# Kernel tuning notes

Hardware: AMD Instinct MI355X
Metric: run time of the kernel (lower is better)

Reference implementation:

```python
import jax, jax.numpy as jnp
import numpy as np

D = 128  # h_dim == in_dim

def _gat_layer(h, d, src, dst, n_dst, W, U, V, a):
    # h: [N_src, Din], d: [E, 1], src/dst: [E]
    z = h @ W.T          # [N_src, D]
    zi = h @ U.T         # [N_src, D]
    t = d @ V.T          # [E, 1]
    Dh = W.shape[0]
    # attn_fc on concat([z_src, z_dst, t]) split into three partial dots
    e = z[src] @ a[:Dh] + z[dst] @ a[Dh:2 * Dh] + t[:, 0] * a[2 * Dh]
    e = jax.nn.leaky_relu(e)  # [E]
    # segment softmax over incoming edges of each dst node
    m = jax.ops.segment_max(e, dst, num_segments=n_dst)
    ex = jnp.exp(e - m[dst])
    s = jax.ops.segment_sum(ex, dst, num_segments=n_dst)
    alpha = ex / s[dst]  # [E]
    zn = jax.ops.segment_sum(alpha[:, None] * z[src], dst, num_segments=n_dst)
    return jax.nn.relu(zi[:n_dst] + zn)


def setup_inputs() -> dict:
    key = jax.random.key(0)
    ks = jax.random.split(key, 16)
    N0, ND0, ND1 = 100000, 40000, 20000
    E0, E1 = 640000, 320000
    sc = 1.0 / np.sqrt(D)
    inp = {
        "attr": jax.random.normal(ks[0], (N0, D), jnp.float32),
        "d0": jax.random.normal(ks[1], (E0, 1), jnp.float32),
        "d1": jax.random.normal(ks[2], (E1, 1), jnp.float32),
        "src0": jax.random.randint(ks[3], (E0,), 0, N0, jnp.int32),
        "dst0": jax.random.randint(ks[4], (E0,), 0, ND0, jnp.int32),
        "src1": jax.random.randint(ks[5], (E1,), 0, ND0, jnp.int32),
        "dst1": jax.random.randint(ks[6], (E1,), 0, ND1, jnp.int32),
        "n_dst0": ND0,
        "n_dst1": ND1,
        "W0": jax.random.normal(ks[7], (D, D), jnp.float32) * sc,
        "U0": jax.random.normal(ks[8], (D, D), jnp.float32) * sc,
        "V0": jax.random.normal(ks[9], (1, 1), jnp.float32),
        "a0": jax.random.normal(ks[10], (2 * D + 1,), jnp.float32) * sc,
        "W1": jax.random.normal(ks[11], (D, D), jnp.float32) * sc,
        "U1": jax.random.normal(ks[12], (D, D), jnp.float32) * sc,
        "V1": jax.random.normal(ks[13], (1, 1), jnp.float32),
        "a1": jax.random.normal(ks[14], (2 * D + 1,), jnp.float32) * sc,
    }
    return inp


def reference(attr, d0, d1, W0, U0, V0, a0, W1, U1, V1, a1,
              src0, dst0, src1, dst1, n_dst0, n_dst1):
    h = _gat_layer(attr, d0, src0, dst0, n_dst0, W0, U0, V0, a0)
    h = _gat_layer(h, d1, src1, dst1, n_dst1, W1, U1, V1, a1)
    return h
```

## Files before the change

kernel.cpp:

```cpp
#include <hip/hip_runtime.h>
#include <math.h>


#define D 128
#define CSTRIDE 32

typedef __bf16 bf16x8 __attribute__((ext_vector_type(8)));
typedef float f32x4 __attribute__((ext_vector_type(4)));

static __device__ __forceinline__ float lrelu(float x) {
  return x >= 0.f ? x : 0.01f * x;
}
static __device__ __forceinline__ unsigned short f2bf(float v) {
  unsigned int u = __float_as_uint(v);
  u += 0x7fffu + ((u >> 16) & 1u);
  return (unsigned short)(u >> 16);
}
static __device__ __forceinline__ float bf2f(unsigned short b) {
  return __uint_as_float((unsigned int)b << 16);
}

static __device__ __forceinline__ float4 loadV4(const float* p) {
  return *(const float4*)p;
}
static __device__ __forceinline__ float4 loadV4(const unsigned short* p) {
  ushort4 t = *(const ushort4*)p;
  return make_float4(bf2f(t.x), bf2f(t.y), bf2f(t.z), bf2f(t.w));
}
static __device__ __forceinline__ void storeV4(float* p, float4 v) {
  *(float4*)p = v;
}
static __device__ __forceinline__ void storeV4(unsigned short* p, float4 v) {
  ushort4 t;
  t.x = f2bf(v.x);
  t.y = f2bf(v.y);
  t.z = f2bf(v.z);
  t.w = f2bf(v.w);
  *(ushort4*)p = t;
}
static __device__ __forceinline__ void storeZi(float* p, float v) { *p = v; }
static __device__ __forceinline__ void storeZi(unsigned short* p, float v) {
  *p = f2bf(v);
}

static __device__ __forceinline__ int swz(int row, int colb) {
  return row * 256 + (colb ^ ((row & 7) << 4));
}

__global__ __launch_bounds__(256) void cvt4_kernel(
    const float* __restrict__ s0, const float* __restrict__ s1,
    const float* __restrict__ s2, const float* __restrict__ s3,
    __bf16* __restrict__ dst) {
  int idx = blockIdx.x * 256 + threadIdx.x;
  const float* s = (idx < 16384) ? s0
                   : (idx < 32768) ? s1
                   : (idx < 49152) ? s2 : s3;
  dst[idx] = (__bf16)s[idx & 16383];
}

__global__ void zero_int_kernel(int* __restrict__ p, int n) {
  int i = blockIdx.x * 256 + threadIdx.x;
  if (i < n) p[i] = 0;
}

static __device__ __forceinline__ void stageA(const float* A, int rblk,
                                              int rlim, int t,
                                              unsigned char* ldsA) {
  const char* base = (const char*)A + (size_t)rblk * 512;
#pragma unroll
  for (int g = 0; g < 8; ++g) {
    int sb = g * 4096 + t * 16;
    float4 v = make_float4(0.f, 0.f, 0.f, 0.f);
    if (rblk + (sb >> 9) < rlim) v = *(const float4*)(base + sb);
    int db = sb >> 1;
    int row = db >> 8, colb = db & 255;
    ushort4 o;
    o.x = f2bf(v.x);
    o.y = f2bf(v.y);
    o.z = f2bf(v.z);
    o.w = f2bf(v.w);
    *(ushort4*)(&ldsA[swz(row, colb)]) = o;
  }
}
static __device__ __forceinline__ void stageA(const unsigned short* A,
                                              int rblk, int rlim, int t,
                                              unsigned char* ldsA) {
  const char* base = (const char*)A + (size_t)rblk * 256;
#pragma unroll
  for (int g = 0; g < 4; ++g) {
    int bi = g * 4096 + t * 16;
    int row = bi >> 8, colb = bi & 255;
    ushort4 lo = {0, 0, 0, 0}, hi = {0, 0, 0, 0};
    if (rblk + row < rlim) {
      lo = *(const ushort4*)(base + bi);
      hi = *(const ushort4*)(base + bi + 8);
    }
    *(ushort4*)(&ldsA[swz(row, colb)]) = lo;
    *(ushort4*)(&ldsA[swz(row, colb) + 8]) = hi;
  }
}

template <typename AT, typename ZiT>
__global__ __launch_bounds__(256, 3) void gemm_lds(
    const AT* __restrict__ A, const __bf16* __restrict__ Wb,
    const __bf16* __restrict__ Ub, unsigned short* __restrict__ z,
    ZiT* __restrict__ zi, const float* __restrict__ a,
    float* __restrict__ zs, float* __restrict__ zd, int n_wb, int rows,
    int ndst) {
  __shared__ unsigned char lds[49152];
  const int t = threadIdx.x;
  const int blk = blockIdx.x;
  const bool isU = (blk >= n_wb);
  const int rblk = (isU ? blk - n_wb : blk) * 64;
  const int rlim = isU ? ndst : rows;
  const __bf16* B = isU ? Ub : Wb;

#pragma unroll
  for (int g = 0; g < 8; ++g) {
    int bi = g * 4096 + t * 16;
    int row = bi >> 8, colb = bi & 255;
    bf16x8 v = *(const bf16x8*)((const char*)B + bi);
    *(bf16x8*)(&lds[swz(row, colb)]) = v;
  }
  stageA(A, rblk, rlim, t, lds + 32768);
  __syncthreads();

  const int wave = t >> 6;
  const int lane = t & 63;
  const int lm = lane & 15;
  const int lk = lane >> 4;
  const int r0 = rblk + wave * 16;
  if (r0 >= rlim) return;

  bf16x8 af[4];
#pragma unroll
  for (int kt = 0; kt < 4; ++kt) {
    int row = wave * 16 + lm;
    af[kt] = *(const bf16x8*)(&lds[32768 + swz(row, kt * 64 + lk * 16)]);
  }

  f32x4 acc[8];
#pragma unroll
  for (int tt = 0; tt < 8; ++tt) acc[tt] = (f32x4){0.f, 0.f, 0.f, 0.f};
#pragma unroll
  for (int kt = 0; kt < 4; ++kt) {
#pragma unroll
    for (int tt = 0; tt < 8; ++tt) {
      int row = tt * 16 + lm;
      bf16x8 bf = *(const bf16x8*)(&lds[swz(row, kt * 64 + lk * 16)]);
      acc[tt] =
          __builtin_amdgcn_mfma_f32_16x16x32_bf16(af[kt], bf, acc[tt], 0, 0, 0);
    }
  }

  if (!isU) {
#pragma unroll
    for (int tt = 0; tt < 8; ++tt)
#pragma unroll
      for (int rr = 0; rr < 4; ++rr)
        z[(size_t)(r0 + lk * 4 + rr) * D + tt * 16 + lm] = f2bf(acc[tt][rr]);

    float p1[4] = {0.f, 0.f, 0.f, 0.f};
    float p2[4] = {0.f, 0.f, 0.f, 0.f};
#pragma unroll
    for (int tt = 0; tt < 8; ++tt) {
      float a1 = a[tt * 16 + lm];
      float a2 = a[D + tt * 16 + lm];
#pragma unroll
      for (int rr = 0; rr < 4; ++rr) {
        p1[rr] += acc[tt][rr] * a1;
        p2[rr] += acc[tt][rr] * a2;
      }
    }
#pragma unroll
    for (int rr = 0; rr < 4; ++rr) {
#pragma unroll
      for (int o = 1; o < 16; o <<= 1) {
        p1[rr] += __shfl_xor(p1[rr], o);
        p2[rr] += __shfl_xor(p2[rr], o);
      }
      if (lm == 0) {
        zs[r0 + lk * 4 + rr] = p1[rr];
        zd[r0 + lk * 4 + rr] = p2[rr];
      }
    }
  } else {
#pragma unroll
    for (int tt = 0; tt < 8; ++tt)
#pragma unroll
      for (int rr = 0; rr < 4; ++rr)
        storeZi(&zi[(size_t)(r0 + lk * 4 + rr) * D + tt * 16 + lm],
                acc[tt][rr]);
  }
}

__global__ void count_rank_kernel(const int* __restrict__ dst0,
                                  const int* __restrict__ dst1,
                                  int* __restrict__ cnt0,
                                  int* __restrict__ cnt1,
                                  int* __restrict__ rank0,
                                  int* __restrict__ rank1, int q0, int q1) {
  int gid = blockIdx.x * 256 + threadIdx.x;
  const int* dst;
  int* cnt;
  int* rank;
  int i0;
  if (gid < q0) {
    dst = dst0; cnt = cnt0; rank = rank0; i0 = gid * 4;
  } else if (gid < q0 + q1) {
    dst = dst1; cnt = cnt1; rank = rank1; i0 = (gid - q0) * 4;
  } else {
    return;
  }
  int4 d4 = *(const int4*)(dst + i0);
  int4 r4;
  r4.x = atomicAdd(&cnt[(size_t)d4.x * CSTRIDE], 1);
  r4.y = atomicAdd(&cnt[(size_t)d4.y * CSTRIDE], 1);
  r4.z = atomicAdd(&cnt[(size_t)d4.z * CSTRIDE], 1);
  r4.w = atomicAdd(&cnt[(size_t)d4.w * CSTRIDE], 1);
  *(int4*)(rank + i0) = r4;
}

__global__ __launch_bounds__(256) void scan_partial2(
    const int* __restrict__ cnt0, const int* __restrict__ cnt1,
    int* __restrict__ part, int nb0, int n0, int n1) {
  __shared__ int sm[4];
  int blk = blockIdx.x;
  const int* cnt;
  int* pt;
  int n, lb;
  if (blk < nb0) {
    cnt = cnt0; pt = part; n = n0; lb = blk;
  } else {
    cnt = cnt1; pt = part + 64; n = n1; lb = blk - nb0;
  }
  int base = lb * 1024;
  int t = threadIdx.x;
  int s = 0;
#pragma unroll
  for (int i = 0; i < 4; ++i) {
    int idx = base + t + i * 256;
    s += (idx < n) ? cnt[(size_t)idx * CSTRIDE] : 0;
  }
  for (int o = 32; o; o >>= 1) s += __shfl_xor(s, o);
  if ((t & 63) == 0) sm[t >> 6] = s;
  __syncthreads();
  if (t == 0) pt[lb] = sm[0] + sm[1] + sm[2] + sm[3];
}

__global__ __launch_bounds__(256) void scan_final2(
    const int* __restrict__ cnt0, const int* __restrict__ cnt1,
    const int* __restrict__ part, int* __restrict__ offs0,
    int* __restrict__ offs1, int nb0, int n0, int n1, int tot0, int tot1) {
  __shared__ int sm[4];
  __shared__ int sbase;
  int blk = blockIdx.x;
  const int* cnt;
  const int* pt;
  int* offs;
  int n, lb, total;
  if (blk < nb0) {
    cnt = cnt0; pt = part; offs = offs0; n = n0; lb = blk; total = tot0;
  } else {
    cnt = cnt1; pt = part + 64; offs = offs1; n = n1; lb = blk - nb0;
    total = tot1;
  }
  int base = lb * 1024;
  int t = threadIdx.x;
  if (t < 64) {
    int v = (t < lb) ? pt[t] : 0;
#pragma unroll
    for (int o = 32; o; o >>= 1) v += __shfl_xor(v, o);
    if (t == 0) sbase = v;
  }
  int idx = base + t * 4;
  int c0 = (idx + 0 < n) ? cnt[(size_t)(idx + 0) * CSTRIDE] : 0;
  int c1 = (idx + 1 < n) ? cnt[(size_t)(idx + 1) * CSTRIDE] : 0;
  int c2 = (idx + 2 < n) ? cnt[(size_t)(idx + 2) * CSTRIDE] : 0;
  int c3 = (idx + 3 < n) ? cnt[(size_t)(idx + 3) * CSTRIDE] : 0;
  int ts = c0 + c1 + c2 + c3;
  int v = ts;
#pragma unroll
  for (int o = 1; o < 64; o <<= 1) {
    int u = __shfl_up(v, o);
    if ((t & 63) >= o) v += u;
  }
  if ((t & 63) == 63) sm[t >> 6] = v;
  __syncthreads();
  int w = t >> 6;
  int waveoff = 0;
  if (w > 0) waveoff += sm[0];
  if (w > 1) waveoff += sm[1];
  if (w > 2) waveoff += sm[2];
  int run = v - ts + waveoff + sbase;
  if (idx + 0 < n) { offs[idx + 0] = run; run += c0; }
  if (idx + 1 < n) { offs[idx + 1] = run; run += c1; }
  if (idx + 2 < n) { offs[idx + 2] = run; run += c2; }
  if (idx + 3 < n) { offs[idx + 3] = run; run += c3; }
  if (lb == 0 && t == 0) offs[n] = total;
}

__global__ void scatter_w_kernel(const int* __restrict__ src,
                                 const int* __restrict__ dst,
                                 const float* __restrict__ dE,
                                 const float* __restrict__ zs,
                                 const float* __restrict__ zd,
                                 const float* __restrict__ V,
                                 const float* __restrict__ a,
                                 const int* __restrict__ rank,
                                 const int* __restrict__ offs,
                                 int2* __restrict__ csr, int E) {
  int i0 = (blockIdx.x * 256 + threadIdx.x) * 4;
  float vc = V[0] * a[2 * D];
  if (i0 + 4 <= E) {
    int4 s4 = *(const int4*)(src + i0);
    int4 d4 = *(const int4*)(dst + i0);
    float4 de = *(const float4*)(dE + i0);
    int4 r4 = *(const int4*)(rank + i0);
    float zs0 = zs[s4.x], zs1 = zs[s4.y], zs2 = zs[s4.z], zs3 = zs[s4.w];
    float zd0 = zd[d4.x], zd1 = zd[d4.y], zd2 = zd[d4.z], zd3 = zd[d4.w];
    int p0 = offs[d4.x] + r4.x;
    int p1 = offs[d4.y] + r4.y;
    int p2 = offs[d4.z] + r4.z;
    int p3 = offs[d4.w] + r4.w;
    float w0 = __expf(lrelu(zs0 + zd0 + de.x * vc));
    float w1 = __expf(lrelu(zs1 + zd1 + de.y * vc));
    float w2 = __expf(lrelu(zs2 + zd2 + de.z * vc));
    float w3 = __expf(lrelu(zs3 + zd3 + de.w * vc));
    csr[p0] = make_int2(s4.x, __float_as_int(w0));
    csr[p1] = make_int2(s4.y, __float_as_int(w1));
    csr[p2] = make_int2(s4.z, __float_as_int(w2));
    csr[p3] = make_int2(s4.w, __float_as_int(w3));
  } else {
    for (int i = i0; i < E; ++i) {
      int di = dst[i];
      int pp = offs[di] + rank[i];
      float w = __expf(lrelu(zs[src[i]] + zd[di] + dE[i] * vc));
      csr[pp] = make_int2(src[i], __float_as_int(w));
    }
  }
}

template <typename OT>
__global__ __launch_bounds__(256) void gat_perdst(
    const unsigned short* __restrict__ z, const int2* __restrict__ csr,
    const int* __restrict__ offs, const OT* __restrict__ ziin,
    OT* __restrict__ hout, int nd) {
  int n = blockIdx.x * 8 + (threadIdx.x >> 5);
  if (n >= nd) return;
  int lane = threadIdx.x & 31;
  int beg = offs[n], end = offs[n + 1];

  float s0 = 0.f, s1 = 0.f;
  float4 acc0 = make_float4(0.f, 0.f, 0.f, 0.f);
  float4 acc1 = make_float4(0.f, 0.f, 0.f, 0.f);
  const unsigned short* zp = z + lane * 4;
  int j = beg;
  for (; j + 8 <= end; j += 8) {
    int2 pr[8];
#pragma unroll
    for (int u = 0; u < 8; ++u) pr[u] = csr[j + u];
    float4 zv[8];
#pragma unroll
    for (int u = 0; u < 8; ++u) zv[u] = loadV4(zp + (size_t)pr[u].x * D);
#pragma unroll
    for (int u = 0; u < 8; u += 2) {
      float wa = __int_as_float(pr[u].y);
      float wb = __int_as_float(pr[u + 1].y);
      s0 += wa;
      acc0.x += wa * zv[u].x;
      acc0.y += wa * zv[u].y;
      acc0.z += wa * zv[u].z;
      acc0.w += wa * zv[u].w;
      s1 += wb;
      acc1.x += wb * zv[u + 1].x;
      acc1.y += wb * zv[u + 1].y;
      acc1.z += wb * zv[u + 1].z;
      acc1.w += wb * zv[u + 1].w;
    }
  }
  for (; j < end; ++j) {
    int2 pr = csr[j];
    float w = __int_as_float(pr.y);
    float4 zv = loadV4(zp + (size_t)pr.x * D);
    s0 += w;
    acc0.x += w * zv.x;
    acc0.y += w * zv.y;
    acc0.z += w * zv.z;
    acc0.w += w * zv.w;
  }
  float s = s0 + s1;
  float inv = (s > 0.f) ? 1.f / s : 0.f;
  float4 acc = make_float4(acc0.x + acc1.x, acc0.y + acc1.y, acc0.z + acc1.z,
                           acc0.w + acc1.w);
  float4 ziv = loadV4(ziin + (size_t)n * D + lane * 4);
  float4 o4;
  o4.x = fmaxf(ziv.x + acc.x * inv, 0.f);
  o4.y = fmaxf(ziv.y + acc.y * inv, 0.f);
  o4.z = fmaxf(ziv.z + acc.z * inv, 0.f);
  o4.w = fmaxf(ziv.w + acc.w * inv, 0.f);
  storeV4(hout + (size_t)n * D + lane * 4, o4);
}

extern "C" void kernel_launch(void* const* d_in, const int* in_sizes, int n_in,
                              void* d_out, int out_size, void* d_ws,
                              size_t ws_size, hipStream_t stream) {
  const float* attr = (const float*)d_in[0];
  const float* d0 = (const float*)d_in[1];
  const float* d1 = (const float*)d_in[2];
  const int* src0 = (const int*)d_in[3];
  const int* dst0 = (const int*)d_in[4];
  const int* src1 = (const int*)d_in[5];
  const int* dst1 = (const int*)d_in[6];
  const float* W0 = (const float*)d_in[9];
  const float* U0 = (const float*)d_in[10];
  const float* V0 = (const float*)d_in[11];
  const float* a0 = (const float*)d_in[12];
  const float* W1 = (const float*)d_in[13];
  const float* U1 = (const float*)d_in[14];
  const float* V1 = (const float*)d_in[15];
  const float* a1 = (const float*)d_in[16];

  const int N0 = in_sizes[0] / D;
  const int E0 = in_sizes[1];
  const int E1 = in_sizes[2];
  const int ND0 = 40000;
  const int ND1 = 20000;

  char* p = (char*)d_ws;
  auto alloc = [&](size_t bytes) {
    char* q = p;
    p += (bytes + 255) & ~(size_t)255;
    return q;
  };
  unsigned short* z = (unsigned short*)alloc((size_t)N0 * D * 2);
  int2* csr = (int2*)alloc((size_t)E0 * 8);
  unsigned short* h1b = (unsigned short*)alloc((size_t)ND0 * D * 2);
  int* rank0 = (int*)alloc((size_t)E0 * 4);
  int* rank1 = (int*)alloc((size_t)E1 * 4);
  float* zs = (float*)alloc((size_t)N0 * 4);
  float* zd = (float*)alloc((size_t)N0 * 4);
  int* offs0 = (int*)alloc((size_t)(ND0 + 1) * 4);
  int* offs1 = (int*)alloc((size_t)(ND1 + 1) * 4);
  int* cnt01 = (int*)alloc((size_t)(ND0 + ND1) * CSTRIDE * 4);
  int* part = (int*)alloc((size_t)128 * 4);
  __bf16* wb = (__bf16*)alloc((size_t)4 * D * D * 2);
  int* cnt0 = cnt01;
  int* cnt1 = cnt01 + (size_t)ND0 * CSTRIDE;
  (void)n_in;
  (void)out_size;
  (void)ws_size;

  float* out = (float*)d_out;

  cvt4_kernel<<<256, 256, 0, stream>>>(W0, U0, W1, U1, wb);
  {
    int ztot = (ND0 + ND1) * CSTRIDE;
    zero_int_kernel<<<(ztot + 255) / 256, 256, 0, stream>>>(cnt01, ztot);
  }
  {
    int q0 = E0 / 4, q1 = E1 / 4;
    count_rank_kernel<<<(q0 + q1 + 255) / 256, 256, 0, stream>>>(
        dst0, dst1, cnt0, cnt1, rank0, rank1, q0, q1);
    int nb0 = (ND0 + 1023) / 1024;
    int nb1 = (ND1 + 1023) / 1024;
    scan_partial2<<<nb0 + nb1, 256, 0, stream>>>(cnt0, cnt1, part, nb0, ND0,
                                                 ND1);
    scan_final2<<<nb0 + nb1, 256, 0, stream>>>(cnt0, cnt1, part, offs0, offs1,
                                               nb0, ND0, ND1, E0, E1);
  }
  const __bf16* W0b = wb;
  const __bf16* U0b = wb + 16384;
  const __bf16* W1b = wb + 32768;
  const __bf16* U1b = wb + 49152;

  {
    int n_wb = (N0 + 63) / 64, n_ub = (ND0 + 63) / 64;
    gemm_lds<float, unsigned short><<<n_wb + n_ub, 256, 0, stream>>>(
        attr, W0b, U0b, z, (unsigned short*)d_out, a0, zs, zd, n_wb, N0, ND0);
  }
  scatter_w_kernel<<<(E0 / 4 + 255) / 256, 256, 0, stream>>>(
      src0, dst0, d0, zs, zd, V0, a0, rank0, offs0, csr, E0);
  gat_perdst<unsigned short><<<(ND0 + 7) / 8, 256, 0, stream>>>(
      z, csr, offs0, (const unsigned short*)d_out, h1b, ND0);

  {
    int n_wb = (ND0 + 63) / 64, n_ub = (ND1 + 63) / 64;
    gemm_lds<unsigned short, float><<<n_wb + n_ub, 256, 0, stream>>>(
        h1b, W1b, U1b, z, out, a1, zs, zd, n_wb, ND0, ND1);
  }
  scatter_w_kernel<<<(E1 / 4 + 255) / 256, 256, 0, stream>>>(
      src1, dst1, d1, zs, zd, V1, a1, rank1, offs1, csr, E1);
  gat_perdst<float><<<(ND1 + 7) / 8, 256, 0, stream>>>(z, csr, offs1, out, out,
                                                       ND1);
}
```

Baseline: 172.9 us.

## Use per-XCD count planes with workgroup-scope atomics for CSR build

Replaces the padded global counter array, one counter per 32-int stride, with eight per-XCD counter planes indexed by the hardware XCC id. Atomics are issued at workgroup scope, and each rank is tagged with the XCD id in its high bits. The scan now sums across planes and writes per-node, per-XCD prefix offsets, which scatter uses to compute final positions. This aims to cut cross-die atomic traffic and coherence cost. In exchange the scan and scatter do extra loads, and correctness relies on all blocks of a workgroup-scope atomic sharing an XCD's L2.

New measurement: 177.6 us. 1.03x slower.

```diff
diff --git a/kernel.cpp b/kernel.cpp
--- a/kernel.cpp
+++ b/kernel.cpp
@@ -3,7 +3,7 @@
 
 
 #define D 128
-#define CSTRIDE 32
+#define NXCD 8
 
 typedef __bf16 bf16x8 __attribute__((ext_vector_type(8)));
 typedef float f32x4 __attribute__((ext_vector_type(4)));
@@ -199,26 +199,44 @@
                                   int* __restrict__ cnt0,
                                   int* __restrict__ cnt1,
                                   int* __restrict__ rank0,
-                                  int* __restrict__ rank1, int q0, int q1) {
+                                  int* __restrict__ rank1, int q0, int q1,
+                                  int nd0, int nd1) {
   int gid = blockIdx.x * 256 + threadIdx.x;
   const int* dst;
   int* cnt;
   int* rank;
-  int i0;
+  int i0, nd;
   if (gid < q0) {
-    dst = dst0; cnt = cnt0; rank = rank0; i0 = gid * 4;
+    dst = dst0; cnt = cnt0; rank = rank0; i0 = gid * 4; nd = nd0;
   } else if (gid < q0 + q1) {
-    dst = dst1; cnt = cnt1; rank = rank1; i0 = (gid - q0) * 4;
+    dst = dst1; cnt = cnt1; rank = rank1; i0 = (gid - q0) * 4; nd = nd1;
   } else {
     return;
   }
+  unsigned xcc;
+  asm("s_getreg_b32 %0, hwreg(HW_REG_XCC_ID)" : "=s"(xcc));
+  xcc &= (NXCD - 1);
+  int* plane = cnt + (size_t)xcc * nd;
+  int hi = (int)(xcc << 27);
   int4 d4 = *(const int4*)(dst + i0);
   int4 r4;
-  r4.x = atomicAdd(&cnt[(size_t)d4.x * CSTRIDE], 1);
-  r4.y = atomicAdd(&cnt[(size_t)d4.y * CSTRIDE], 1);
-  r4.z = atomicAdd(&cnt[(size_t)d4.z * CSTRIDE], 1);
-  r4.w = atomicAdd(&cnt[(size_t)d4.w * CSTRIDE], 1);
+  r4.x = __hip_atomic_fetch_add(&plane[d4.x], 1, __ATOMIC_RELAXED,
+                                __HIP_MEMORY_SCOPE_WORKGROUP) | hi;
+  r4.y = __hip_atomic_fetch_add(&plane[d4.y], 1, __ATOMIC_RELAXED,
+                                __HIP_MEMORY_SCOPE_WORKGROUP) | hi;
+  r4.z = __hip_atomic_fetch_add(&plane[d4.z], 1, __ATOMIC_RELAXED,
+                                __HIP_MEMORY_SCOPE_WORKGROUP) | hi;
+  r4.w = __hip_atomic_fetch_add(&plane[d4.w], 1, __ATOMIC_RELAXED,
+                                __HIP_MEMORY_SCOPE_WORKGROUP) | hi;
   *(int4*)(rank + i0) = r4;
+}
+
+static __device__ __forceinline__ int node_total(const int* cnt, int node,
+                                                 int nd) {
+  int s = 0;
+#pragma unroll
+  for (int x = 0; x < NXCD; ++x) s += cnt[(size_t)x * nd + node];
+  return s;
 }
 
 __global__ __launch_bounds__(256) void scan_partial2(
@@ -240,7 +258,7 @@
 #pragma unroll
   for (int i = 0; i < 4; ++i) {
     int idx = base + t + i * 256;
-    s += (idx < n) ? cnt[(size_t)idx * CSTRIDE] : 0;
+    if (idx < n) s += node_total(cnt, idx, n);
   }
   for (int o = 32; o; o >>= 1) s += __shfl_xor(s, o);
   if ((t & 63) == 0) sm[t >> 6] = s;
@@ -251,18 +269,21 @@
 __global__ __launch_bounds__(256) void scan_final2(
     const int* __restrict__ cnt0, const int* __restrict__ cnt1,
     const int* __restrict__ part, int* __restrict__ offs0,
-    int* __restrict__ offs1, int nb0, int n0, int n1, int tot0, int tot1) {
+    int* __restrict__ offs1, int* __restrict__ px0, int* __restrict__ px1,
+    int nb0, int n0, int n1, int tot0, int tot1) {
   __shared__ int sm[4];
   __shared__ int sbase;
   int blk = blockIdx.x;
   const int* cnt;
   const int* pt;
   int* offs;
+  int* px;
   int n, lb, total;
   if (blk < nb0) {
-    cnt = cnt0; pt = part; offs = offs0; n = n0; lb = blk; total = tot0;
+    cnt = cnt0; pt = part; offs = offs0; px = px0; n = n0; lb = blk;
+    total = tot0;
   } else {
-    cnt = cnt1; pt = part + 64; offs = offs1; n = n1; lb = blk - nb0;
+    cnt = cnt1; pt = part + 64; offs = offs1; px = px1; n = n1; lb = blk - nb0;
     total = tot1;
   }
   int base = lb * 1024;
@@ -274,11 +295,21 @@
     if (t == 0) sbase = v;
   }
   int idx = base + t * 4;
-  int c0 = (idx + 0 < n) ? cnt[(size_t)(idx + 0) * CSTRIDE] : 0;
-  int c1 = (idx + 1 < n) ? cnt[(size_t)(idx + 1) * CSTRIDE] : 0;
-  int c2 = (idx + 2 < n) ? cnt[(size_t)(idx + 2) * CSTRIDE] : 0;
-  int c3 = (idx + 3 < n) ? cnt[(size_t)(idx + 3) * CSTRIDE] : 0;
-  int ts = c0 + c1 + c2 + c3;
+  int c[4] = {0, 0, 0, 0};
+#pragma unroll
+  for (int k = 0; k < 4; ++k) {
+    int node = idx + k;
+    if (node < n) {
+      int run = 0;
+#pragma unroll
+      for (int x = 0; x < NXCD; ++x) {
+        px[(size_t)node * NXCD + x] = run;
+        run += cnt[(size_t)x * n + node];
+      }
+      c[k] = run;
+    }
+  }
+  int ts = c[0] + c[1] + c[2] + c[3];
   int v = ts;
 #pragma unroll
   for (int o = 1; o < 64; o <<= 1) {
@@ -293,10 +324,10 @@
   if (w > 1) waveoff += sm[1];
   if (w > 2) waveoff += sm[2];
   int run = v - ts + waveoff + sbase;
-  if (idx + 0 < n) { offs[idx + 0] = run; run += c0; }
-  if (idx + 1 < n) { offs[idx + 1] = run; run += c1; }
-  if (idx + 2 < n) { offs[idx + 2] = run; run += c2; }
-  if (idx + 3 < n) { offs[idx + 3] = run; run += c3; }
+  if (idx + 0 < n) { offs[idx + 0] = run; run += c[0]; }
+  if (idx + 1 < n) { offs[idx + 1] = run; run += c[1]; }
+  if (idx + 2 < n) { offs[idx + 2] = run; run += c[2]; }
+  if (idx + 3 < n) { offs[idx + 3] = run; run += c[3]; }
   if (lb == 0 && t == 0) offs[n] = total;
 }
 
@@ -309,9 +340,11 @@
                                  const float* __restrict__ a,
                                  const int* __restrict__ rank,
                                  const int* __restrict__ offs,
+                                 const int* __restrict__ px,
                                  int2* __restrict__ csr, int E) {
   int i0 = (blockIdx.x * 256 + threadIdx.x) * 4;
   float vc = V[0] * a[2 * D];
+  const int LMASK = (1 << 27) - 1;
   if (i0 + 4 <= E) {
     int4 s4 = *(const int4*)(src + i0);
     int4 d4 = *(const int4*)(dst + i0);
@@ -319,10 +352,14 @@
     int4 r4 = *(const int4*)(rank + i0);
     float zs0 = zs[s4.x], zs1 = zs[s4.y], zs2 = zs[s4.z], zs3 = zs[s4.w];
     float zd0 = zd[d4.x], zd1 = zd[d4.y], zd2 = zd[d4.z], zd3 = zd[d4.w];
-    int p0 = offs[d4.x] + r4.x;
-    int p1 = offs[d4.y] + r4.y;
-    int p2 = offs[d4.z] + r4.z;
-    int p3 = offs[d4.w] + r4.w;
+    int p0 = offs[d4.x] + px[(size_t)d4.x * NXCD + ((unsigned)r4.x >> 27)] +
+             (r4.x & LMASK);
+    int p1 = offs[d4.y] + px[(size_t)d4.y * NXCD + ((unsigned)r4.y >> 27)] +
+             (r4.y & LMASK);
+    int p2 = offs[d4.z] + px[(size_t)d4.z * NXCD + ((unsigned)r4.z >> 27)] +
+             (r4.z & LMASK);
+    int p3 = offs[d4.w] + px[(size_t)d4.w * NXCD + ((unsigned)r4.w >> 27)] +
+             (r4.w & LMASK);
     float w0 = __expf(lrelu(zs0 + zd0 + de.x * vc));
     float w1 = __expf(lrelu(zs1 + zd1 + de.y * vc));
     float w2 = __expf(lrelu(zs2 + zd2 + de.z * vc));
@@ -334,7 +371,9 @@
   } else {
     for (int i = i0; i < E; ++i) {
       int di = dst[i];
-      int pp = offs[di] + rank[i];
+      int r = rank[i];
+      int pp = offs[di] + px[(size_t)di * NXCD + ((unsigned)r >> 27)] +
+               (r & LMASK);
       float w = __expf(lrelu(zs[src[i]] + zd[di] + dE[i] * vc));
       csr[pp] = make_int2(src[i], __float_as_int(w));
     }
@@ -442,11 +481,13 @@
   float* zd = (float*)alloc((size_t)N0 * 4);
   int* offs0 = (int*)alloc((size_t)(ND0 + 1) * 4);
   int* offs1 = (int*)alloc((size_t)(ND1 + 1) * 4);
-  int* cnt01 = (int*)alloc((size_t)(ND0 + ND1) * CSTRIDE * 4);
+  int* cnt01 = (int*)alloc((size_t)(ND0 + ND1) * NXCD * 4);
+  int* px0 = (int*)alloc((size_t)ND0 * NXCD * 4);
+  int* px1 = (int*)alloc((size_t)ND1 * NXCD * 4);
   int* part = (int*)alloc((size_t)128 * 4);
   __bf16* wb = (__bf16*)alloc((size_t)4 * D * D * 2);
   int* cnt0 = cnt01;
-  int* cnt1 = cnt01 + (size_t)ND0 * CSTRIDE;
+  int* cnt1 = cnt01 + (size_t)ND0 * NXCD;
   (void)n_in;
   (void)out_size;
   (void)ws_size;
@@ -455,19 +496,20 @@
 
   cvt4_kernel<<<256, 256, 0, stream>>>(W0, U0, W1, U1, wb);
   {
-    int ztot = (ND0 + ND1) * CSTRIDE;
+    int ztot = (ND0 + ND1) * NXCD;
     zero_int_kernel<<<(ztot + 255) / 256, 256, 0, stream>>>(cnt01, ztot);
   }
   {
     int q0 = E0 / 4, q1 = E1 / 4;
     count_rank_kernel<<<(q0 + q1 + 255) / 256, 256, 0, stream>>>(
-        dst0, dst1, cnt0, cnt1, rank0, rank1, q0, q1);
+        dst0, dst1, cnt0, cnt1, rank0, rank1, q0, q1, ND0, ND1);
     int nb0 = (ND0 + 1023) / 1024;
     int nb1 = (ND1 + 1023) / 1024;
     scan_partial2<<<nb0 + nb1, 256, 0, stream>>>(cnt0, cnt1, part, nb0, ND0,
                                                  ND1);
     scan_final2<<<nb0 + nb1, 256, 0, stream>>>(cnt0, cnt1, part, offs0, offs1,
-                                               nb0, ND0, ND1, E0, E1);
+                                               px0, px1, nb0, ND0, ND1, E0,
+                                               E1);
   }
   const __bf16* W0b = wb;
   const __bf16* U0b = wb + 16384;
@@ -480,7 +522,7 @@
         attr, W0b, U0b, z, (unsigned short*)d_out, a0, zs, zd, n_wb, N0, ND0);
   }
   scatter_w_kernel<<<(E0 / 4 + 255) / 256, 256, 0, stream>>>(
-      src0, dst0, d0, zs, zd, V0, a0, rank0, offs0, csr, E0);
+      src0, dst0, d0, zs, zd, V0, a0, rank0, offs0, px0, csr, E0);
   gat_perdst<unsigned short><<<(ND0 + 7) / 8, 256, 0, stream>>>(
       z, csr, offs0, (const unsigned short*)d_out, h1b, ND0);
 
@@ -490,7 +532,7 @@
         h1b, W1b, U1b, z, out, a1, zs, zd, n_wb, ND0, ND1);
   }
   scatter_w_kernel<<<(E1 / 4 + 255) / 256, 256, 0, stream>>>(
-      src1, dst1, d1, zs, zd, V1, a1, rank1, offs1, csr, E1);
+      src1, dst1, d1, zs, zd, V1, a1, rank1, offs1, px1, csr, E1);
   gat_perdst<float><<<(ND1 + 7) / 8, 256, 0, stream>>>(z, csr, offs1, out, out,
                                                        ND1);
 }
```
